# Kernel optimization log

Hardware: AMD Instinct MI355X
Metric: run time of the kernel (lower is better)

## Reference

```python
import jax, jax.numpy as jnp
import numpy as np

H_DIM = 768
N_HEADS = 12
SEQ = 4096
MLP_RATIO = 4
EPS = 1e-5


def layernorm(x, g, b):
    mu = jnp.mean(x, axis=-1, keepdims=True)
    var = jnp.var(x, axis=-1, keepdims=True)
    return (x - mu) * jax.lax.rsqrt(var + EPS) * g + b


def setup_inputs() -> dict:
    key = jax.random.key(0)
    ks = jax.random.split(key, 16)
    C, F = H_DIM, MLP_RATIO * H_DIM
    s = 1.0 / np.sqrt(C)
    inp = {
        "x": jax.random.normal(ks[0], (1, SEQ, C), dtype=jnp.float32),
        "Wq": jax.random.normal(ks[1], (C, C), dtype=jnp.float32) * s,
        "bq": jnp.zeros((C,), jnp.float32),
        "Wk": jax.random.normal(ks[2], (C, C), dtype=jnp.float32) * s,
        "bk": jnp.zeros((C,), jnp.float32),
        "Wv": jax.random.normal(ks[3], (C, C), dtype=jnp.float32) * s,
        "bv": jnp.zeros((C,), jnp.float32),
        "Wo": jax.random.normal(ks[4], (C, C), dtype=jnp.float32) * s,
        "bo": jnp.zeros((C,), jnp.float32),
        "ln1_g": jnp.ones((C,), jnp.float32),
        "ln1_b": jnp.zeros((C,), jnp.float32),
        "W1": jax.random.normal(ks[5], (C, F), dtype=jnp.float32) * s,
        "b1": jnp.zeros((F,), jnp.float32),
        "W2": jax.random.normal(ks[6], (F, C), dtype=jnp.float32) * (1.0 / np.sqrt(F)),
        "b2": jnp.zeros((C,), jnp.float32),
        "ln2_g": jnp.ones((C,), jnp.float32),
        "ln2_b": jnp.zeros((C,), jnp.float32),
    }
    return inp


def reference(x, Wq, bq, Wk, bk, Wv, bv, Wo, bo, ln1_g, ln1_b, W1, b1, W2, b2, ln2_g, ln2_b):
    B, T, C = x.shape
    N, D = N_HEADS, C // N_HEADS

    # --- masked self-attention (naive, materializes T x T scores) ---
    q = (x @ Wq + bq).reshape(B, T, N, D).transpose(0, 2, 1, 3)  # [B,N,T,D]
    k = (x @ Wk + bk).reshape(B, T, N, D).transpose(0, 2, 1, 3)
    v = (x @ Wv + bv).reshape(B, T, N, D).transpose(0, 2, 1, 3)

    logits = jnp.einsum("bntd,bnsd->bnts", q, k) / jnp.sqrt(jnp.float32(D))
    causal = jnp.tril(jnp.ones((T, T), dtype=bool))  # True where allowed
    logits = jnp.where(causal, logits, -jnp.inf)
    attn = jax.nn.softmax(logits, axis=-1)
    out = jnp.einsum("bnts,bnsd->bntd", attn, v)
    out = out.transpose(0, 2, 1, 3).reshape(B, T, C)
    attn_out = out @ Wo + bo

    # --- post-norm residual + MLP ---
    h = layernorm(x + attn_out, ln1_g, ln1_b)
    mlp = jax.nn.gelu(h @ W1 + b1, approximate=False) @ W2 + b2
    y = layernorm(h + mlp, ln2_g, ln2_b)
    return y
```

## Files before the change

### kernel.cpp

```cpp
#include <hip/hip_runtime.h>
#include <hip/hip_bf16.h>
#include <math.h>

#define T_SEQ 4096
#define C_DIM 768
#define N_HEADS 12
#define D_HEAD 64
#define F_DIM 3072
#define EPS 1e-5f
#define QSCALE 0.18033688011112042f

typedef __attribute__((ext_vector_type(8))) short short8;
typedef __attribute__((ext_vector_type(4))) float f32x4;

__device__ __forceinline__ void gload_lds16(const void* g, void* lds) {
    __builtin_amdgcn_global_load_lds(
        (const __attribute__((address_space(1))) unsigned int*)g,
        (__attribute__((address_space(3))) unsigned int*)lds, 16, 0, 0);
}

__launch_bounds__(256)
__global__ void prep_all(const float* __restrict__ Wq, const float* __restrict__ Wk,
                         const float* __restrict__ Wv, const float* __restrict__ Wo,
                         const float* __restrict__ W1, const float* __restrict__ W2,
                         const float* __restrict__ x,
                         const float* __restrict__ bq, const float* __restrict__ bk,
                         const float* __restrict__ bv,
                         __hip_bfloat16* __restrict__ Wqkv_t, __hip_bfloat16* __restrict__ Wo_t,
                         __hip_bfloat16* __restrict__ W1_t, __hip_bfloat16* __restrict__ W2_t,
                         __hip_bfloat16* __restrict__ xb, float* __restrict__ bqkv) {
    const int b = blockIdx.x;
    const int tid = threadIdx.x;
    if (b < 1728) {
        __shared__ float tile[64][65];
        const float* W; __hip_bfloat16* Wt; int K, N, kx, ny;
        if (b < 576) {
            const int z = b / 144, t = b % 144;
            kx = t % 12; ny = t / 12; K = C_DIM; N = C_DIM;
            W  = (z == 0) ? Wq : (z == 1) ? Wk : (z == 2) ? Wv : Wo;
            Wt = (z < 3) ? (Wqkv_t + (size_t)z * C_DIM * C_DIM) : Wo_t;
        } else if (b < 1152) {
            const int t = b - 576; kx = t % 12; ny = t / 12;
            K = C_DIM; N = F_DIM; W = W1; Wt = W1_t;
        } else {
            const int t = b - 1152; kx = t % 48; ny = t / 48;
            K = F_DIM; N = C_DIM; W = W2; Wt = W2_t;
        }
        const int k0 = kx * 64, n0 = ny * 64;
        const int c = tid & 63, r0 = (tid >> 6) * 16;
        #pragma unroll
        for (int i = 0; i < 16; ++i)
            tile[r0 + i][c] = W[(size_t)(k0 + r0 + i) * N + n0 + c];
        __syncthreads();
        #pragma unroll
        for (int i = 0; i < 16; ++i)
            Wt[(size_t)(n0 + r0 + i) * K + k0 + c] = __float2bfloat16(tile[c][r0 + i]);
    } else if (b < 4800) {
        const int i = (b - 1728) * 256 + tid;
        const float4 v = *reinterpret_cast<const float4*>(&x[(size_t)i * 4]);
        ushort4 u;
        u.x = __bfloat16_as_ushort(__float2bfloat16(v.x));
        u.y = __bfloat16_as_ushort(__float2bfloat16(v.y));
        u.z = __bfloat16_as_ushort(__float2bfloat16(v.z));
        u.w = __bfloat16_as_ushort(__float2bfloat16(v.w));
        *reinterpret_cast<ushort4*>(&xb[(size_t)i * 4]) = u;
    } else {
        const int i = (b - 4800) * 256 + tid;
        if (i < C_DIM) {
            bqkv[i] = bq[i];
            bqkv[C_DIM + i] = bk[i];
            bqkv[2 * C_DIM + i] = bv[i];
        }
    }
}

__launch_bounds__(256)
__global__ void transpose_v(const __hip_bfloat16* __restrict__ V,
                            __hip_bfloat16* __restrict__ Vt) {
    __shared__ __hip_bfloat16 tile[64][65];
    const int t0 = blockIdx.x * 64;
    const int c0 = blockIdx.y * 64;
    const int tid = threadIdx.x;
    const int c = tid & 63;
    const int r0 = (tid >> 6) * 16;
    #pragma unroll
    for (int i = 0; i < 16; ++i)
        tile[r0 + i][c] = V[(size_t)(t0 + r0 + i) * C_DIM + c0 + c];
    __syncthreads();
    #pragma unroll
    for (int i = 0; i < 16; ++i)
        Vt[(size_t)(c0 + r0 + i) * T_SEQ + t0 + c] = tile[c][r0 + i];
}

#define GBK 64

template<int MODE, int TM, int TN, int SPLITK, bool SWZ>
__launch_bounds__(256)
__global__ void gemm_mfma(const __hip_bfloat16* __restrict__ A,
                          const __hip_bfloat16* __restrict__ Bt,
                          const float* __restrict__ bias,
                          float* __restrict__ outf,
                          __hip_bfloat16* __restrict__ outq,
                          __hip_bfloat16* __restrict__ outk,
                          __hip_bfloat16* __restrict__ outv,
                          int M, int N, int K) {
    constexpr int WM = TM / 2, WN = TN / 2;
    constexpr int FM = WM / 16, FN = WN / 16;
    constexpr int AISS = TM / 32, BISS = TN / 32;

    __shared__ __hip_bfloat16 As[TM][GBK];
    __shared__ __hip_bfloat16 Bs[TN][GBK];

    const int tid = threadIdx.x;
    const int l   = tid & 63;
    const int w   = tid >> 6;
    const int lr  = l & 15;
    const int lg  = l >> 4;
    const int wr  = w >> 1;
    const int wc  = w & 1;

    int bid = blockIdx.y * gridDim.x + blockIdx.x;
    if constexpr (SWZ) {
        const int nwg = gridDim.x * gridDim.y;
        const int cpx = nwg >> 3;
        bid = (bid & 7) * cpx + (bid >> 3);
    }
    const int bm = (bid / gridDim.x) * TM;
    const int bn = (bid % gridDim.x) * TN;

    const int kz   = (SPLITK > 1) ? blockIdx.z : 0;
    const int kbeg = kz * (K / SPLITK);
    const int kend = kbeg + K / SPLITK;

    const int srow  = l >> 3;
    const int skoff = (l & 7) * 8;

    f32x4 acc[FM][FN];
    #pragma unroll
    for (int m = 0; m < FM; ++m)
        #pragma unroll
        for (int n = 0; n < FN; ++n)
            acc[m][n] = {0.f, 0.f, 0.f, 0.f};

    for (int k0 = kbeg; k0 < kend; k0 += GBK) {
        if (k0 != kbeg) __syncthreads();
        #pragma unroll
        for (int i = 0; i < AISS; ++i) {
            const int rb = (w * AISS + i) * 8;
            gload_lds16(&A[(size_t)(bm + rb + srow) * K + k0 + skoff], &As[rb][0]);
        }
        #pragma unroll
        for (int i = 0; i < BISS; ++i) {
            const int rb = (w * BISS + i) * 8;
            gload_lds16(&Bt[(size_t)(bn + rb + srow) * K + k0 + skoff], &Bs[rb][0]);
        }
        __syncthreads();

        #pragma unroll
        for (int kk = 0; kk < 2; ++kk) {
            short8 af[FM], bf[FN];
            #pragma unroll
            for (int m = 0; m < FM; ++m)
                af[m] = *reinterpret_cast<const short8*>(
                    &As[wr * WM + m * 16 + lr][kk * 32 + lg * 8]);
            #pragma unroll
            for (int n = 0; n < FN; ++n)
                bf[n] = *reinterpret_cast<const short8*>(
                    &Bs[wc * WN + n * 16 + lr][kk * 32 + lg * 8]);
            #pragma unroll
            for (int m = 0; m < FM; ++m)
                #pragma unroll
                for (int n = 0; n < FN; ++n)
                    acc[m][n] = __builtin_amdgcn_mfma_f32_16x16x32_bf16(af[m], bf[n], acc[m][n], 0, 0, 0);
        }
    }

    #pragma unroll
    for (int m = 0; m < FM; ++m) {
        #pragma unroll
        for (int rr = 0; rr < 4; ++rr) {
            const int row = bm + wr * WM + m * 16 + lg * 4 + rr;
            #pragma unroll
            for (int n = 0; n < FN; ++n) {
                const int col = bn + wc * WN + n * 16 + lr;
                float v = acc[m][n][rr] + ((SPLITK == 1 || kz == 0) ? bias[col] : 0.f);
                if constexpr (MODE == 0) {
                    outf[(size_t)kz * M * N + (size_t)row * N + col] = v;
                } else if constexpr (MODE == 1) {
                    v = 0.5f * v * (1.0f + erff(v * 0.70710678118654752f));
                    outq[(size_t)row * N + col] = __float2bfloat16(v);
                } else {
                    if (col < C_DIM)
                        outq[(size_t)row * C_DIM + col] = __float2bfloat16(v * QSCALE);
                    else if (col < 2 * C_DIM)
                        outk[(size_t)row * C_DIM + (col - C_DIM)] = __float2bfloat16(v);
                    else
                        outv[(size_t)row * C_DIM + (col - 2 * C_DIM)] = __float2bfloat16(v);
                }
            }
        }
    }
}

#define QBLK 64
#define KVB 128

__launch_bounds__(256)
__global__ void attn_mfma(const __hip_bfloat16* __restrict__ q,
                          const __hip_bfloat16* __restrict__ k,
                          const __hip_bfloat16* __restrict__ vt,
                          __hip_bfloat16* __restrict__ o) {
    __shared__ __hip_bfloat16 Ks[2][KVB][64];
    __shared__ __hip_bfloat16 Vts[2][D_HEAD][KVB];
    __shared__ __hip_bfloat16 Ps[4][16][KVB];

    const int tid  = threadIdx.x;
    const int wid  = tid >> 6;
    const int lane = tid & 63;
    const int lr   = lane & 15;
    const int lg   = lane >> 4;

    const int h  = blockIdx.x;
    const int q0 = T_SEQ - QBLK - blockIdx.y * QBLK;
    const int qw = q0 + wid * 16;

    const int ksrc = 8 * ((lane & 7) ^ (lane >> 3));
    const int kr   = lane >> 3;
    const int vr   = lane >> 4;
    const int vs   = lane & 15;

    short8 aq[2];
    #pragma unroll
    for (int kk = 0; kk < 2; ++kk)
        aq[kk] = *reinterpret_cast<const short8*>(
            &q[(size_t)(qw + lr) * C_DIM + h * D_HEAD + kk * 32 + lg * 8]);

    f32x4 o_acc[4];
    #pragma unroll
    for (int dc = 0; dc < 4; ++dc) o_acc[dc] = {0.f, 0.f, 0.f, 0.f};
    float m_run[4], l_part[4];
    #pragma unroll
    for (int r = 0; r < 4; ++r) { m_run[r] = -1e30f; l_part[r] = 0.f; }

    auto stage = [&](int buf, int s0) {
        #pragma unroll
        for (int i = 0; i < 4; ++i) {
            const int rb = wid * 32 + i * 8;
            gload_lds16(&k[(size_t)(s0 + rb + kr) * C_DIM + h * D_HEAD + ksrc],
                        &Ks[buf][rb][0]);
        }
        #pragma unroll
        for (int i = 0; i < 4; ++i) {
            const int vb = wid * 16 + i * 4;
            const int vsrc = 8 * (vs ^ (i * 4 + vr));
            gload_lds16(&vt[(size_t)(h * D_HEAD + vb + vr) * T_SEQ + s0 + vsrc],
                        &Vts[buf][vb][0]);
        }
    };

    const int n_tiles = (q0 + QBLK + KVB - 1) / KVB;

    stage(0, 0);
    __syncthreads();

    for (int t = 0; t < n_tiles; ++t) {
        const int cur = t & 1;
        if (t + 1 < n_tiles) stage(cur ^ 1, (t + 1) * KVB);

        f32x4 s_acc[8];
        __builtin_amdgcn_s_setprio(1);
        #pragma unroll
        for (int c = 0; c < 8; ++c) {
            s_acc[c] = {0.f, 0.f, 0.f, 0.f};
            #pragma unroll
            for (int kk = 0; kk < 2; ++kk) {
                const short8 bk8 = *reinterpret_cast<const short8*>(
                    &Ks[cur][c * 16 + lr][8 * ((4 * kk + lg) ^ (lr & 7))]);
                s_acc[c] = __builtin_amdgcn_mfma_f32_16x16x32_bf16(aq[kk], bk8, s_acc[c], 0, 0, 0);
            }
        }
        __builtin_amdgcn_s_setprio(0);

        if (t == n_tiles - 1) {
            const int s0 = t * KVB;
            #pragma unroll
            for (int c = 0; c < 8; ++c)
                #pragma unroll
                for (int r = 0; r < 4; ++r) {
                    const int sg = s0 + c * 16 + lr;
                    const int qg = qw + lg * 4 + r;
                    if (sg > qg) s_acc[c][r] = -1e30f;
                }
        }

        float pm[4];
        #pragma unroll
        for (int r = 0; r < 4; ++r) {
            const float m0 = fmaxf(fmaxf(s_acc[0][r], s_acc[1][r]),
                                   fmaxf(s_acc[2][r], s_acc[3][r]));
            const float m1 = fmaxf(fmaxf(s_acc[4][r], s_acc[5][r]),
                                   fmaxf(s_acc[6][r], s_acc[7][r]));
            pm[r] = fmaxf(m0, m1);
        }
        const float need = fmaxf(fmaxf(pm[0] - m_run[0], pm[1] - m_run[1]),
                                 fmaxf(pm[2] - m_run[2], pm[3] - m_run[3]));
        if (!__all(need <= 8.0f)) {
            #pragma unroll
            for (int r = 0; r < 4; ++r) {
                float nm = pm[r];
                #pragma unroll
                for (int off = 1; off < 16; off <<= 1)
                    nm = fmaxf(nm, __shfl_xor(nm, off));
                nm = fmaxf(nm, m_run[r]);
                const float corr = __builtin_amdgcn_exp2f(m_run[r] - nm);
                m_run[r] = nm;
                l_part[r] *= corr;
                #pragma unroll
                for (int dc = 0; dc < 4; ++dc) o_acc[dc][r] *= corr;
            }
        }
        #pragma unroll
        for (int r = 0; r < 4; ++r) {
            const int qrow = lg * 4 + r;
            float ls = 0.f;
            #pragma unroll
            for (int c = 0; c < 8; ++c) {
                const float pv = __builtin_amdgcn_exp2f(s_acc[c][r] - m_run[r]);
                ls += pv;
                const int slot = (2 * c + (lr >> 3)) ^ qrow;
                Ps[wid][qrow][slot * 8 + (lr & 7)] = __float2bfloat16(pv);
            }
            l_part[r] += ls;
        }

        short8 ap[4];
        #pragma unroll
        for (int kk = 0; kk < 4; ++kk)
            ap[kk] = *reinterpret_cast<const short8*>(
                &Ps[wid][lr][8 * ((4 * kk + lg) ^ lr)]);
        __builtin_amdgcn_s_setprio(1);
        #pragma unroll
        for (int dc = 0; dc < 4; ++dc)
            #pragma unroll
            for (int kk = 0; kk < 4; ++kk) {
                const short8 bv8 = *reinterpret_cast<const short8*>(
                    &Vts[cur][dc * 16 + lr][8 * ((4 * kk + lg) ^ lr)]);
                o_acc[dc] = __builtin_amdgcn_mfma_f32_16x16x32_bf16(ap[kk], bv8, o_acc[dc], 0, 0, 0);
            }
        __builtin_amdgcn_s_setprio(0);

        __syncthreads();
    }

    #pragma unroll
    for (int r = 0; r < 4; ++r) {
        #pragma unroll
        for (int off = 1; off < 16; off <<= 1)
            l_part[r] += __shfl_xor(l_part[r], off);
    }

    #pragma unroll
    for (int dc = 0; dc < 4; ++dc)
        #pragma unroll
        for (int r = 0; r < 4; ++r)
            o[(size_t)(qw + lg * 4 + r) * C_DIM + h * D_HEAD + dc * 16 + lr] =
                __float2bfloat16(o_acc[dc][r] / l_part[r]);
}

template<bool WB16>
__launch_bounds__(256)
__global__ void add_ln(const float* __restrict__ a, const float* __restrict__ b0,
                       const float* __restrict__ b1,
                       const float* __restrict__ g, const float* __restrict__ beta,
                       float* __restrict__ outf, __hip_bfloat16* __restrict__ outb) {
    const int row = blockIdx.x;
    const int tid = threadIdx.x;
    const size_t rb = (size_t)row * C_DIM;

    float x[3];
    #pragma unroll
    for (int i = 0; i < 3; ++i) {
        const int c = tid + 256 * i;
        x[i] = a[rb + c] + b0[rb + c] + b1[rb + c];
    }

    float s = x[0] + x[1] + x[2];
    float s2 = x[0] * x[0] + x[1] * x[1] + x[2] * x[2];

    #pragma unroll
    for (int off = 32; off; off >>= 1) {
        s  += __shfl_xor(s, off);
        s2 += __shfl_xor(s2, off);
    }

    __shared__ float red[10];
    const int wave = tid >> 6;
    const int lane = tid & 63;
    if (lane == 0) { red[wave] = s; red[4 + wave] = s2; }
    __syncthreads();
    if (tid == 0) {
        const float ts  = red[0] + red[1] + red[2] + red[3];
        const float ts2 = red[4] + red[5] + red[6] + red[7];
        const float mu = ts * (1.0f / C_DIM);
        const float var = ts2 * (1.0f / C_DIM) - mu * mu;
        red[8] = mu;
        red[9] = rsqrtf(var + EPS);
    }
    __syncthreads();
    const float mu = red[8];
    const float rstd = red[9];

    #pragma unroll
    for (int i = 0; i < 3; ++i) {
        const int c = tid + 256 * i;
        const float v = (x[i] - mu) * rstd * g[c] + beta[c];
        outf[rb + c] = v;
        if constexpr (WB16) outb[rb + c] = __float2bfloat16(v);
    }
}

extern "C" void kernel_launch(void* const* d_in, const int* in_sizes, int n_in,
                              void* d_out, int out_size, void* d_ws, size_t ws_size,
                              hipStream_t stream) {
    const float* x     = (const float*)d_in[0];
    const float* Wq    = (const float*)d_in[1];
    const float* bq    = (const float*)d_in[2];
    const float* Wk    = (const float*)d_in[3];
    const float* bk    = (const float*)d_in[4];
    const float* Wv    = (const float*)d_in[5];
    const float* bv    = (const float*)d_in[6];
    const float* Wo    = (const float*)d_in[7];
    const float* bo    = (const float*)d_in[8];
    const float* ln1_g = (const float*)d_in[9];
    const float* ln1_b = (const float*)d_in[10];
    const float* W1    = (const float*)d_in[11];
    const float* b1    = (const float*)d_in[12];
    const float* W2    = (const float*)d_in[13];
    const float* b2    = (const float*)d_in[14];
    const float* ln2_g = (const float*)d_in[15];
    const float* ln2_b = (const float*)d_in[16];

    float* out = (float*)d_out;

    char* wsb = (char*)d_ws;
    const size_t TCb16 = (size_t)T_SEQ * C_DIM * 2;
    const size_t TCf32 = (size_t)T_SEQ * C_DIM * 4;
    __hip_bfloat16* xb  = (__hip_bfloat16*)(wsb);
    __hip_bfloat16* qb  = (__hip_bfloat16*)(wsb + TCb16);
    __hip_bfloat16* kb  = (__hip_bfloat16*)(wsb + 2 * TCb16);
    __hip_bfloat16* vtb = (__hip_bfloat16*)(wsb + 3 * TCb16);
    __hip_bfloat16* mid = (__hip_bfloat16*)(wsb);
    float* proj0 = (float*)(wsb + 4 * TCb16);
    float* proj1 = (float*)(wsb + 4 * TCb16 + TCf32);
    __hip_bfloat16* vb = (__hip_bfloat16*)proj0;
    float* mlpo0 = proj0;
    float* mlpo1 = proj1;
    __hip_bfloat16* obuf = (__hip_bfloat16*)(wsb + 4 * TCb16 + 2 * TCf32);
    __hip_bfloat16* hb   = obuf;
    float* hbuf = (float*)(wsb + 4 * TCb16 + 2 * TCf32 + TCb16);
    char* we = wsb + 4 * TCb16 + 2 * TCf32 + TCb16 + TCf32;
    __hip_bfloat16* Wqkv_t = (__hip_bfloat16*)(we);
    __hip_bfloat16* Wo_t   = (__hip_bfloat16*)(we + 3538944);
    __hip_bfloat16* W1_t   = (__hip_bfloat16*)(we + 3538944 + 1179648);
    __hip_bfloat16* W2_t   = (__hip_bfloat16*)(we + 3538944 + 1179648 + 4718592);
    float* bqkv            = (float*)(we + 3538944 + 1179648 + 2 * 4718592);

    const dim3 blk256(256);

    prep_all<<<dim3(4803), blk256, 0, stream>>>(Wq, Wk, Wv, Wo, W1, W2, x, bq, bk, bv,
                                                Wqkv_t, Wo_t, W1_t, W2_t, xb, bqkv);

    gemm_mfma<2, 128, 128, 1, true><<<dim3(18, 32), blk256, 0, stream>>>(
        xb, Wqkv_t, bqkv, nullptr, qb, kb, vb, T_SEQ, 3 * C_DIM, C_DIM);

    transpose_v<<<dim3(T_SEQ / 64, C_DIM / 64), blk256, 0, stream>>>(vb, vtb);

    attn_mfma<<<dim3(N_HEADS, T_SEQ / QBLK), blk256, 0, stream>>>(qb, kb, vtb, obuf);

    gemm_mfma<0, 64, 64, 2, false><<<dim3(12, 64, 2), blk256, 0, stream>>>(
        obuf, Wo_t, bo, proj0, nullptr, nullptr, nullptr, T_SEQ, C_DIM, C_DIM);

    add_ln<true><<<dim3(T_SEQ), blk256, 0, stream>>>(x, proj0, proj1, ln1_g, ln1_b, hbuf, hb);

    gemm_mfma<1, 128, 128, 1, true><<<dim3(24, 32), blk256, 0, stream>>>(
        hb, W1_t, b1, nullptr, mid, nullptr, nullptr, T_SEQ, F_DIM, C_DIM);

    gemm_mfma<0, 64, 64, 2, false><<<dim3(12, 64, 2), blk256, 0, stream>>>(
        mid, W2_t, b2, mlpo0, nullptr, nullptr, nullptr, T_SEQ, C_DIM, F_DIM);

    add_ln<false><<<dim3(T_SEQ), blk256, 0, stream>>>(hbuf, mlpo0, mlpo1, ln2_g, ln2_b, out, nullptr);
}
```

Baseline: 318.6 us.

## Restructure attention to 128-query blocks with 64-key tiles and two row-groups per wave

The attention kernel now gives each wave 32 query rows (two 16-row MFMA groups) instead of 16, and shrinks the KV tile from 128 to 64. Each K/V fragment read from LDS is reused across both row groups, halving per-query K/V staging traffic and grid size. Causal masking now covers the last two tiles. The output-projection and W2 GEMMs also switch to a 128x64 tile with half the grid rows. Costs are more registers per wave, fewer blocks for the GPU to schedule, and coarser causal load balance.

```diff
diff --git a/kernel.cpp b/kernel.cpp
--- a/kernel.cpp
+++ b/kernel.cpp
@@ -202,8 +202,8 @@
     }
 }
 
-#define QBLK 64
-#define KVB 128
+#define QBLK 128
+#define KVB 64
 
 __launch_bounds__(256)
 __global__ void attn_mfma(const __hip_bfloat16* __restrict__ q,
@@ -212,7 +212,7 @@
                           __hip_bfloat16* __restrict__ o) {
     __shared__ __hip_bfloat16 Ks[2][KVB][64];
     __shared__ __hip_bfloat16 Vts[2][D_HEAD][KVB];
-    __shared__ __hip_bfloat16 Ps[4][16][KVB];
+    __shared__ __hip_bfloat16 Ps[4][32][KVB];
 
     const int tid  = threadIdx.x;
     const int wid  = tid >> 6;
@@ -222,43 +222,46 @@
 
     const int h  = blockIdx.x;
     const int q0 = T_SEQ - QBLK - blockIdx.y * QBLK;
-    const int qw = q0 + wid * 16;
-
-    const int ksrc = 8 * ((lane & 7) ^ (lane >> 3));
-    const int kr   = lane >> 3;
-    const int vr   = lane >> 4;
-    const int vs   = lane & 15;
-
-    short8 aq[2];
-    #pragma unroll
-    for (int kk = 0; kk < 2; ++kk)
-        aq[kk] = *reinterpret_cast<const short8*>(
-            &q[(size_t)(qw + lr) * C_DIM + h * D_HEAD + kk * 32 + lg * 8]);
-
-    f32x4 o_acc[4];
-    #pragma unroll
-    for (int dc = 0; dc < 4; ++dc) o_acc[dc] = {0.f, 0.f, 0.f, 0.f};
-    float m_run[4], l_part[4];
-    #pragma unroll
-    for (int r = 0; r < 4; ++r) { m_run[r] = -1e30f; l_part[r] = 0.f; }
+    const int qw = q0 + wid * 32;
+
+    const int src8 = 8 * ((lane & 7) ^ (lane >> 3));
+    const int r8   = lane >> 3;
+
+    short8 aq[2][2];
+    #pragma unroll
+    for (int m = 0; m < 2; ++m)
+        #pragma unroll
+        for (int kk = 0; kk < 2; ++kk)
+            aq[m][kk] = *reinterpret_cast<const short8*>(
+                &q[(size_t)(qw + m * 16 + lr) * C_DIM + h * D_HEAD + kk * 32 + lg * 8]);
+
+    f32x4 o_acc[2][4];
+    #pragma unroll
+    for (int m = 0; m < 2; ++m)
+        #pragma unroll
+        for (int dc = 0; dc < 4; ++dc) o_acc[m][dc] = {0.f, 0.f, 0.f, 0.f};
+    float m_run[2][4], l_part[2][4];
+    #pragma unroll
+    for (int m = 0; m < 2; ++m)
+        #pragma unroll
+        for (int r = 0; r < 4; ++r) { m_run[m][r] = -1e30f; l_part[m][r] = 0.f; }
 
     auto stage = [&](int buf, int s0) {
         #pragma unroll
-        for (int i = 0; i < 4; ++i) {
-            const int rb = wid * 32 + i * 8;
-            gload_lds16(&k[(size_t)(s0 + rb + kr) * C_DIM + h * D_HEAD + ksrc],
+        for (int i = 0; i < 2; ++i) {
+            const int rb = wid * 16 + i * 8;
+            gload_lds16(&k[(size_t)(s0 + rb + r8) * C_DIM + h * D_HEAD + src8],
                         &Ks[buf][rb][0]);
         }
         #pragma unroll
-        for (int i = 0; i < 4; ++i) {
-            const int vb = wid * 16 + i * 4;
-            const int vsrc = 8 * (vs ^ (i * 4 + vr));
-            gload_lds16(&vt[(size_t)(h * D_HEAD + vb + vr) * T_SEQ + s0 + vsrc],
+        for (int i = 0; i < 2; ++i) {
+            const int vb = wid * 16 + i * 8;
+            gload_lds16(&vt[(size_t)(h * D_HEAD + vb + r8) * T_SEQ + s0 + src8],
                         &Vts[buf][vb][0]);
         }
     };
 
-    const int n_tiles = (q0 + QBLK + KVB - 1) / KVB;
+    const int n_tiles = q0 / KVB + 2;
 
     stage(0, 0);
     __syncthreads();
@@ -267,104 +270,130 @@
         const int cur = t & 1;
         if (t + 1 < n_tiles) stage(cur ^ 1, (t + 1) * KVB);
 
-        f32x4 s_acc[8];
+        f32x4 s_acc[2][4];
         __builtin_amdgcn_s_setprio(1);
         #pragma unroll
-        for (int c = 0; c < 8; ++c) {
-            s_acc[c] = {0.f, 0.f, 0.f, 0.f};
-            #pragma unroll
-            for (int kk = 0; kk < 2; ++kk) {
-                const short8 bk8 = *reinterpret_cast<const short8*>(
+        for (int c = 0; c < 4; ++c) {
+            short8 bk8[2];
+            #pragma unroll
+            for (int kk = 0; kk < 2; ++kk)
+                bk8[kk] = *reinterpret_cast<const short8*>(
                     &Ks[cur][c * 16 + lr][8 * ((4 * kk + lg) ^ (lr & 7))]);
-                s_acc[c] = __builtin_amdgcn_mfma_f32_16x16x32_bf16(aq[kk], bk8, s_acc[c], 0, 0, 0);
+            #pragma unroll
+            for (int m = 0; m < 2; ++m) {
+                s_acc[m][c] = {0.f, 0.f, 0.f, 0.f};
+                #pragma unroll
+                for (int kk = 0; kk < 2; ++kk)
+                    s_acc[m][c] = __builtin_amdgcn_mfma_f32_16x16x32_bf16(
+                        aq[m][kk], bk8[kk], s_acc[m][c], 0, 0, 0);
             }
         }
         __builtin_amdgcn_s_setprio(0);
 
-        if (t == n_tiles - 1) {
+        if (t >= n_tiles - 2) {
             const int s0 = t * KVB;
             #pragma unroll
-            for (int c = 0; c < 8; ++c)
+            for (int m = 0; m < 2; ++m)
+                #pragma unroll
+                for (int c = 0; c < 4; ++c)
+                    #pragma unroll
+                    for (int r = 0; r < 4; ++r) {
+                        const int sg = s0 + c * 16 + lr;
+                        const int qg = qw + m * 16 + lg * 4 + r;
+                        if (sg > qg) s_acc[m][c][r] = -1e30f;
+                    }
+        }
+
+        float pm[2][4];
+        #pragma unroll
+        for (int m = 0; m < 2; ++m)
+            #pragma unroll
+            for (int r = 0; r < 4; ++r)
+                pm[m][r] = fmaxf(fmaxf(s_acc[m][0][r], s_acc[m][1][r]),
+                                 fmaxf(s_acc[m][2][r], s_acc[m][3][r]));
+        float need = -1e30f;
+        #pragma unroll
+        for (int m = 0; m < 2; ++m)
+            #pragma unroll
+            for (int r = 0; r < 4; ++r)
+                need = fmaxf(need, pm[m][r] - m_run[m][r]);
+        if (!__all(need <= 8.0f)) {
+            #pragma unroll
+            for (int m = 0; m < 2; ++m)
                 #pragma unroll
                 for (int r = 0; r < 4; ++r) {
-                    const int sg = s0 + c * 16 + lr;
-                    const int qg = qw + lg * 4 + r;
-                    if (sg > qg) s_acc[c][r] = -1e30f;
+                    float nm = pm[m][r];
+                    #pragma unroll
+                    for (int off = 1; off < 16; off <<= 1)
+                        nm = fmaxf(nm, __shfl_xor(nm, off));
+                    nm = fmaxf(nm, m_run[m][r]);
+                    const float corr = __builtin_amdgcn_exp2f(m_run[m][r] - nm);
+                    m_run[m][r] = nm;
+                    l_part[m][r] *= corr;
+                    #pragma unroll
+                    for (int dc = 0; dc < 4; ++dc) o_acc[m][dc][r] *= corr;
                 }
         }
-
-        float pm[4];
+        #pragma unroll
+        for (int m = 0; m < 2; ++m)
+            #pragma unroll
+            for (int r = 0; r < 4; ++r) {
+                const int qr = lg * 4 + r;
+                float ls = 0.f;
+                #pragma unroll
+                for (int c = 0; c < 4; ++c) {
+                    const float pv = __builtin_amdgcn_exp2f(s_acc[m][c][r] - m_run[m][r]);
+                    ls += pv;
+                    const int slot = (2 * c + (lr >> 3)) ^ (qr & 7);
+                    Ps[wid][m * 16 + qr][slot * 8 + (lr & 7)] = __float2bfloat16(pv);
+                }
+                l_part[m][r] += ls;
+            }
+
+        short8 ap[2][2];
+        #pragma unroll
+        for (int m = 0; m < 2; ++m)
+            #pragma unroll
+            for (int kk = 0; kk < 2; ++kk)
+                ap[m][kk] = *reinterpret_cast<const short8*>(
+                    &Ps[wid][m * 16 + lr][8 * ((4 * kk + lg) ^ (lr & 7))]);
+        __builtin_amdgcn_s_setprio(1);
+        #pragma unroll
+        for (int dc = 0; dc < 4; ++dc) {
+            short8 bv8[2];
+            #pragma unroll
+            for (int kk = 0; kk < 2; ++kk)
+                bv8[kk] = *reinterpret_cast<const short8*>(
+                    &Vts[cur][dc * 16 + lr][8 * ((4 * kk + lg) ^ (lr & 7))]);
+            #pragma unroll
+            for (int m = 0; m < 2; ++m)
+                #pragma unroll
+                for (int kk = 0; kk < 2; ++kk)
+                    o_acc[m][dc] = __builtin_amdgcn_mfma_f32_16x16x32_bf16(
+                        ap[m][kk], bv8[kk], o_acc[m][dc], 0, 0, 0);
+        }
+        __builtin_amdgcn_s_setprio(0);
+
+        __syncthreads();
+    }
+
+    #pragma unroll
+    for (int m = 0; m < 2; ++m)
         #pragma unroll
         for (int r = 0; r < 4; ++r) {
-            const float m0 = fmaxf(fmaxf(s_acc[0][r], s_acc[1][r]),
-                                   fmaxf(s_acc[2][r], s_acc[3][r]));
-            const float m1 = fmaxf(fmaxf(s_acc[4][r], s_acc[5][r]),
-                                   fmaxf(s_acc[6][r], s_acc[7][r]));
-            pm[r] = fmaxf(m0, m1);
-        }
-        const float need = fmaxf(fmaxf(pm[0] - m_run[0], pm[1] - m_run[1]),
-                                 fmaxf(pm[2] - m_run[2], pm[3] - m_run[3]));
-        if (!__all(need <= 8.0f)) {
-            #pragma unroll
-            for (int r = 0; r < 4; ++r) {
-                float nm = pm[r];
-                #pragma unroll
-                for (int off = 1; off < 16; off <<= 1)
-                    nm = fmaxf(nm, __shfl_xor(nm, off));
-                nm = fmaxf(nm, m_run[r]);
-                const float corr = __builtin_amdgcn_exp2f(m_run[r] - nm);
-                m_run[r] = nm;
-                l_part[r] *= corr;
-                #pragma unroll
-                for (int dc = 0; dc < 4; ++dc) o_acc[dc][r] *= corr;
-            }
-        }
-        #pragma unroll
-        for (int r = 0; r < 4; ++r) {
-            const int qrow = lg * 4 + r;
-            float ls = 0.f;
-            #pragma unroll
-            for (int c = 0; c < 8; ++c) {
-                const float pv = __builtin_amdgcn_exp2f(s_acc[c][r] - m_run[r]);
-                ls += pv;
-                const int slot = (2 * c + (lr >> 3)) ^ qrow;
-                Ps[wid][qrow][slot * 8 + (lr & 7)] = __float2bfloat16(pv);
-            }
-            l_part[r] += ls;
-        }
-
-        short8 ap[4];
-        #pragma unroll
-        for (int kk = 0; kk < 4; ++kk)
-            ap[kk] = *reinterpret_cast<const short8*>(
-                &Ps[wid][lr][8 * ((4 * kk + lg) ^ lr)]);
-        __builtin_amdgcn_s_setprio(1);
+            #pragma unroll
+            for (int off = 1; off < 16; off <<= 1)
+                l_part[m][r] += __shfl_xor(l_part[m][r], off);
+        }
+
+    #pragma unroll
+    for (int m = 0; m < 2; ++m)
         #pragma unroll
         for (int dc = 0; dc < 4; ++dc)
             #pragma unroll
-            for (int kk = 0; kk < 4; ++kk) {
-                const short8 bv8 = *reinterpret_cast<const short8*>(
-                    &Vts[cur][dc * 16 + lr][8 * ((4 * kk + lg) ^ lr)]);
-                o_acc[dc] = __builtin_amdgcn_mfma_f32_16x16x32_bf16(ap[kk], bv8, o_acc[dc], 0, 0, 0);
-            }
-        __builtin_amdgcn_s_setprio(0);
-
-        __syncthreads();
-    }
-
-    #pragma unroll
-    for (int r = 0; r < 4; ++r) {
-        #pragma unroll
-        for (int off = 1; off < 16; off <<= 1)
-            l_part[r] += __shfl_xor(l_part[r], off);
-    }
-
-    #pragma unroll
-    for (int dc = 0; dc < 4; ++dc)
-        #pragma unroll
-        for (int r = 0; r < 4; ++r)
-            o[(size_t)(qw + lg * 4 + r) * C_DIM + h * D_HEAD + dc * 16 + lr] =
-                __float2bfloat16(o_acc[dc][r] / l_part[r]);
+            for (int r = 0; r < 4; ++r)
+                o[(size_t)(qw + m * 16 + lg * 4 + r) * C_DIM + h * D_HEAD + dc * 16 + lr] =
+                    __float2bfloat16(o_acc[m][dc][r] / l_part[m][r]);
 }
 
 template<bool WB16>
@@ -477,7 +506,7 @@
 
     attn_mfma<<<dim3(N_HEADS, T_SEQ / QBLK), blk256, 0, stream>>>(qb, kb, vtb, obuf);
 
-    gemm_mfma<0, 64, 64, 2, false><<<dim3(12, 64, 2), blk256, 0, stream>>>(
+    gemm_mfma<0, 128, 64, 2, false><<<dim3(12, 32, 2), blk256, 0, stream>>>(
         obuf, Wo_t, bo, proj0, nullptr, nullptr, nullptr, T_SEQ, C_DIM, C_DIM);
 
     add_ln<true><<<dim3(T_SEQ), blk256, 0, stream>>>(x, proj0, proj1, ln1_g, ln1_b, hbuf, hb);
@@ -485,7 +514,7 @@
     gemm_mfma<1, 128, 128, 1, true><<<dim3(24, 32), blk256, 0, stream>>>(
         hb, W1_t, b1, nullptr, mid, nullptr, nullptr, T_SEQ, F_DIM, C_DIM);
 
-    gemm_mfma<0, 64, 64, 2, false><<<dim3(12, 64, 2), blk256, 0, stream>>>(
+    gemm_mfma<0, 128, 64, 2, false><<<dim3(12, 32, 2), blk256, 0, stream>>>(
         mid, W2_t, b2, mlpo0, nullptr, nullptr, nullptr, T_SEQ, C_DIM, F_DIM);
 
     add_ln<false><<<dim3(T_SEQ), blk256, 0, stream>>>(hbuf, mlpo0, mlpo1, ln2_g, ln2_b, out, nullptr);
```

Result: slower. 361.2 us (+13.4%).
